# Performance work log

Measured on AMD Instinct MI355X. Metric: run time of the kernel, lower is better.

## Reference

```python
import jax, jax.numpy as jnp
import numpy as np


def _resize_bilinear_align_corners(x, out_size):
    # x: [B, C, h, w] -> [B, C, out_size, out_size], matches F.interpolate(mode='bilinear', align_corners=True)
    def axis_interp(arr, size_in, size_out, axis):
        coords = jnp.linspace(0.0, size_in - 1.0, size_out)
        i0 = jnp.floor(coords).astype(jnp.int32)
        i1 = jnp.minimum(i0 + 1, size_in - 1)
        t = (coords - i0).astype(arr.dtype)
        a0 = jnp.take(arr, i0, axis=axis)
        a1 = jnp.take(arr, i1, axis=axis)
        shape = [1] * arr.ndim
        shape[axis] = size_out
        t = t.reshape(shape)
        return a0 * (1.0 - t) + a1 * t

    B, C, h, w = x.shape
    x = axis_interp(x, h, out_size, 2)
    x = axis_interp(x, w, out_size, 3)
    return x


def _similarity_matrix(x, sp, num):
    # Torch: mean_values[i][j] = mean(x[i][sp_repeated[i] == j], dim=0)
    # Boolean indexing flattens across channels, so this is a SCALAR mean over
    # (channels x segment pixels), broadcast to all C channels.
    B, C, H, W = x.shape
    xs = x.sum(axis=1).reshape(B, H * W)          # sum over channels, per pixel
    ids = sp.reshape(B, H * W)
    seg_sum = jax.vmap(
        lambda v, i: jax.ops.segment_sum(v, i, num_segments=num))(xs, ids)
    cnt = jax.vmap(
        lambda i: jax.ops.segment_sum(jnp.ones(i.shape, x.dtype), i,
                                      num_segments=num))(ids)
    m = seg_sum / (cnt * C)                        # [B, num] scalar mean per segment
    # diff vector over channels has identical entries -> norm(diff)/sqrt(C) == |m_i - m_j|
    return 1.0 - jnp.abs(m[:, :, None] - m[:, None, :])  # [B, num, num]


def reference(input, feature, sp, num):
    feature = _resize_bilinear_align_corners(feature, input.shape[-1])
    mat1 = _similarity_matrix(input, sp, num)
    mat2 = _similarity_matrix(feature, sp, num)
    return jnp.mean(jnp.abs(mat1 - mat2))


def setup_inputs() -> dict:
    key = jax.random.key(0)
    k1, k2, k3 = jax.random.split(key, 3)
    B, C_in, H, W = 8, 64, 256, 256
    C_feat, hf, wf = 256, 64, 64
    num = 256
    return {
        "input": jax.random.normal(k1, (B, C_in, H, W), dtype=jnp.float32),
        "feature": jax.random.normal(k2, (B, C_feat, hf, wf), dtype=jnp.float32),
        "sp": jax.random.randint(k3, (B, 1, H, W), 0, num, dtype=jnp.int32),
        "num": num,
    }
```

## Files before the change

### kernel.cpp

```cpp
#include <hip/hip_runtime.h>

#define NB 8
#define C_IN 64
#define HW 65536
#define CF 256
#define FHW 4096
#define NSEG 256


__global__ void featsum_kernel(const float* __restrict__ feat,
                               float* __restrict__ featsum) {
    int b = blockIdx.y, cg = blockIdx.z;
    int p = blockIdx.x * 256 + threadIdx.x;
    const float* f = feat + ((size_t)(b * CF + cg * 32)) * FHW + p;
    float s = 0.f;
#pragma unroll
    for (int c = 0; c < 32; ++c) s += f[(size_t)c * FHW];
    atomicAdd(&featsum[b * FHW + p], s);
}

__global__ __launch_bounds__(256) void main_kernel(
    const float* __restrict__ input, const int* __restrict__ sp,
    const float* __restrict__ featsum, float* __restrict__ seg) {
    __shared__ float fls[FHW];
    __shared__ float bin_in[NSEG], bin_feat[NSEG], bin_cnt[NSEG];
    int b = blockIdx.y;
    int t = threadIdx.x;
    for (int i = t; i < FHW; i += 256) fls[i] = featsum[b * FHW + i];
    bin_in[t] = 0.f; bin_feat[t] = 0.f; bin_cnt[t] = 0.f;
    __syncthreads();

    int p0 = blockIdx.x * 1024 + t * 4;
    int v0 = p0 >> 2;
    const float4* in4 = (const float4*)(input + (size_t)b * C_IN * HW);
    float4 xs = make_float4(0.f, 0.f, 0.f, 0.f);
#pragma unroll
    for (int c = 0; c < C_IN; ++c) {
        float4 v = in4[(size_t)c * (HW / 4) + v0];
        xs.x += v.x; xs.y += v.y; xs.z += v.z; xs.w += v.w;
    }
    int4 sv = ((const int4*)(sp + (size_t)b * HW))[v0];

    int y = p0 >> 8;
    float cy = (float)y * (63.0f / 255.0f);
    int iy = (int)cy; float ty = cy - (float)iy; int iy1 = min(iy + 1, 63);
    float xsv[4] = {xs.x, xs.y, xs.z, xs.w};
    int   ssv[4] = {sv.x, sv.y, sv.z, sv.w};
#pragma unroll
    for (int k = 0; k < 4; ++k) {
        int x = (p0 + k) & 255;
        float cx = (float)x * (63.0f / 255.0f);
        int ix = (int)cx; float tx = cx - (float)ix; int ix1 = min(ix + 1, 63);
        float f00 = fls[iy * 64 + ix],  f10 = fls[iy1 * 64 + ix];
        float f01 = fls[iy * 64 + ix1], f11 = fls[iy1 * 64 + ix1];
        float a0 = f00 * (1.f - ty) + f10 * ty;
        float a1 = f01 * (1.f - ty) + f11 * ty;
        float fs = a0 * (1.f - tx) + a1 * tx;
        int s = ssv[k];
        atomicAdd(&bin_in[s], xsv[k]);
        atomicAdd(&bin_feat[s], fs);
        atomicAdd(&bin_cnt[s], 1.f);
    }
    __syncthreads();
    atomicAdd(&seg[b * NSEG + t], bin_in[t]);
    atomicAdd(&seg[NB * NSEG + b * NSEG + t], bin_feat[t]);
    atomicAdd(&seg[2 * NB * NSEG + b * NSEG + t], bin_cnt[t]);
}

__global__ void pair_kernel(const float* __restrict__ seg,
                            float* __restrict__ pp) {
    __shared__ float m1[NSEG], m2[NSEG];
    __shared__ float wsum[4];
    int b = blockIdx.y, ig = blockIdx.x, t = threadIdx.x;
    float cnt = seg[2 * NB * NSEG + b * NSEG + t];
    m1[t] = seg[b * NSEG + t] / (cnt * 64.0f);
    m2[t] = seg[NB * NSEG + b * NSEG + t] / (cnt * 256.0f);
    __syncthreads();
    int i = ig * 64 + (t & 63);
    int j0 = (t >> 6) * 64;
    float a1 = m1[i], a2 = m2[i];
    float acc = 0.f;
#pragma unroll 8
    for (int jj = 0; jj < 64; ++jj) {
        int j = j0 + jj;
        acc += fabsf(fabsf(a1 - m1[j]) - fabsf(a2 - m2[j]));
    }
    for (int off = 32; off; off >>= 1) acc += __shfl_down(acc, off);
    if ((t & 63) == 0) wsum[t >> 6] = acc;
    __syncthreads();
    if (t == 0) pp[b * 4 + ig] = wsum[0] + wsum[1] + wsum[2] + wsum[3];
}

__global__ void final_kernel(const float* __restrict__ pp,
                             float* __restrict__ out) {
    int t = threadIdx.x;
    float v = (t < 32) ? pp[t] : 0.f;
    for (int off = 32; off; off >>= 1) v += __shfl_down(v, off);
    if (t == 0) out[0] = v / 524288.0f;
}

extern "C" void kernel_launch(void* const* d_in, const int* in_sizes, int n_in,
                              void* d_out, int out_size, void* d_ws, size_t ws_size,
                              hipStream_t stream) {
    const float* input   = (const float*)d_in[0];
    const float* feature = (const float*)d_in[1];
    const int*   sp      = (const int*)d_in[2];
    float* ws = (float*)d_ws;
    float* featsum = ws;
    float* seg     = ws + NB * FHW;
    float* pp      = seg + 3 * NB * NSEG;

    hipMemsetAsync(d_ws, 0, (size_t)(NB * FHW + 3 * NB * NSEG + 32) * sizeof(float), stream);
    featsum_kernel<<<dim3(16, 8, 8), 256, 0, stream>>>(feature, featsum);
    main_kernel<<<dim3(64, 8), 256, 0, stream>>>(input, sp, featsum, seg);
    pair_kernel<<<dim3(4, 8), 256, 0, stream>>>(seg, pp);
    final_kernel<<<1, 64, 0, stream>>>(pp, (float*)d_out);
}
```

Before: 52.89 us.

## Replace global atomics and memset with per-block partial buffers reduced downstream

Global atomicAdd accumulation is replaced with plain stores of per-group and per-block partial results, which removes the hipMemsetAsync launch. The feature channel-sum kernel now loads float4 and writes 8 channel-group partials, and main_kernel adds those partials together when it fills shared memory. main_kernel writes per-block segment bins, and a single 1024-thread pair block per batch reduces the 64 block partials before computing the pairwise term. The cost is redundant partial reads in each main block and more serial reduction work in pair_kernel.

```diff
diff --git a/kernel.cpp b/kernel.cpp
--- a/kernel.cpp
+++ b/kernel.cpp
@@ -6,32 +6,46 @@
 #define CF 256
 #define FHW 4096
 #define NSEG 256
+#define NGRP 8
+#define MBLK 64
 
 
 __global__ void featsum_kernel(const float* __restrict__ feat,
-                               float* __restrict__ featsum) {
-    int b = blockIdx.y, cg = blockIdx.z;
-    int p = blockIdx.x * 256 + threadIdx.x;
-    const float* f = feat + ((size_t)(b * CF + cg * 32)) * FHW + p;
-    float s = 0.f;
+                               float* __restrict__ partial) {
+    int b = blockIdx.y, g = blockIdx.z;
+    int q = blockIdx.x * 256 + threadIdx.x;
+    const float4* f4 = (const float4*)(feat + ((size_t)(b * CF + g * 32)) * FHW);
+    float4 s = make_float4(0.f, 0.f, 0.f, 0.f);
 #pragma unroll
-    for (int c = 0; c < 32; ++c) s += f[(size_t)c * FHW];
-    atomicAdd(&featsum[b * FHW + p], s);
+    for (int c = 0; c < 32; ++c) {
+        float4 v = f4[(size_t)c * (FHW / 4) + q];
+        s.x += v.x; s.y += v.y; s.z += v.z; s.w += v.w;
+    }
+    ((float4*)partial)[(size_t)(b * NGRP + g) * (FHW / 4) + q] = s;
 }
 
 __global__ __launch_bounds__(256) void main_kernel(
     const float* __restrict__ input, const int* __restrict__ sp,
-    const float* __restrict__ featsum, float* __restrict__ seg) {
+    const float* __restrict__ partial, float* __restrict__ seg_part) {
     __shared__ float fls[FHW];
-    __shared__ float bin_in[NSEG], bin_feat[NSEG], bin_cnt[NSEG];
+    __shared__ float bin[3][NSEG];
     int b = blockIdx.y;
     int t = threadIdx.x;
-    for (int i = t; i < FHW; i += 256) fls[i] = featsum[b * FHW + i];
-    bin_in[t] = 0.f; bin_feat[t] = 0.f; bin_cnt[t] = 0.f;
+    const float4* p4 = (const float4*)(partial + (size_t)b * NGRP * FHW);
+    for (int i = t; i < FHW / 4; i += 256) {
+        float4 s = p4[i];
+#pragma unroll
+        for (int g = 1; g < NGRP; ++g) {
+            float4 v = p4[g * (FHW / 4) + i];
+            s.x += v.x; s.y += v.y; s.z += v.z; s.w += v.w;
+        }
+        ((float4*)fls)[i] = s;
+    }
+    bin[0][t] = 0.f; bin[1][t] = 0.f; bin[2][t] = 0.f;
     __syncthreads();
 
     int p0 = blockIdx.x * 1024 + t * 4;
-    int v0 = p0 >> 2;
+    int v0 = blockIdx.x * 256 + t;
     const float4* in4 = (const float4*)(input + (size_t)b * C_IN * HW);
     float4 xs = make_float4(0.f, 0.f, 0.f, 0.f);
 #pragma unroll
@@ -57,27 +71,39 @@
         float a1 = f01 * (1.f - ty) + f11 * ty;
         float fs = a0 * (1.f - tx) + a1 * tx;
         int s = ssv[k];
-        atomicAdd(&bin_in[s], xsv[k]);
-        atomicAdd(&bin_feat[s], fs);
-        atomicAdd(&bin_cnt[s], 1.f);
+        atomicAdd(&bin[0][s], xsv[k]);
+        atomicAdd(&bin[1][s], fs);
+        atomicAdd(&bin[2][s], 1.f);
     }
     __syncthreads();
-    atomicAdd(&seg[b * NSEG + t], bin_in[t]);
-    atomicAdd(&seg[NB * NSEG + b * NSEG + t], bin_feat[t]);
-    atomicAdd(&seg[2 * NB * NSEG + b * NSEG + t], bin_cnt[t]);
+    float* sb = seg_part + (size_t)(b * MBLK + blockIdx.x) * 3 * NSEG;
+    sb[t]            = bin[0][t];
+    sb[NSEG + t]     = bin[1][t];
+    sb[2 * NSEG + t] = bin[2][t];
 }
 
-__global__ void pair_kernel(const float* __restrict__ seg,
-                            float* __restrict__ pp) {
+__global__ __launch_bounds__(1024) void pair_kernel(
+    const float* __restrict__ seg_part, float* __restrict__ pp) {
+    __shared__ float s3[3 * NSEG];
     __shared__ float m1[NSEG], m2[NSEG];
-    __shared__ float wsum[4];
-    int b = blockIdx.y, ig = blockIdx.x, t = threadIdx.x;
-    float cnt = seg[2 * NB * NSEG + b * NSEG + t];
-    m1[t] = seg[b * NSEG + t] / (cnt * 64.0f);
-    m2[t] = seg[NB * NSEG + b * NSEG + t] / (cnt * 256.0f);
+    __shared__ float red[16];
+    int b = blockIdx.x, t = threadIdx.x;
+    if (t < 3 * NSEG) {
+        float s = 0.f;
+        const float* base = seg_part + (size_t)b * MBLK * 3 * NSEG + t;
+#pragma unroll 8
+        for (int k = 0; k < MBLK; ++k) s += base[(size_t)k * 3 * NSEG];
+        s3[t] = s;
+    }
     __syncthreads();
-    int i = ig * 64 + (t & 63);
-    int j0 = (t >> 6) * 64;
+    if (t < NSEG) {
+        float cnt = s3[2 * NSEG + t];
+        m1[t] = s3[t] / (cnt * 64.0f);
+        m2[t] = s3[NSEG + t] / (cnt * 256.0f);
+    }
+    __syncthreads();
+    int i = t & 255;
+    int j0 = (t >> 8) * 64;
     float a1 = m1[i], a2 = m2[i];
     float acc = 0.f;
 #pragma unroll 8
@@ -85,17 +111,24 @@
         int j = j0 + jj;
         acc += fabsf(fabsf(a1 - m1[j]) - fabsf(a2 - m2[j]));
     }
+#pragma unroll
     for (int off = 32; off; off >>= 1) acc += __shfl_down(acc, off);
-    if ((t & 63) == 0) wsum[t >> 6] = acc;
+    if ((t & 63) == 0) red[t >> 6] = acc;
     __syncthreads();
-    if (t == 0) pp[b * 4 + ig] = wsum[0] + wsum[1] + wsum[2] + wsum[3];
+    if (t == 0) {
+        float s = 0.f;
+#pragma unroll
+        for (int w = 0; w < 16; ++w) s += red[w];
+        pp[b] = s;
+    }
 }
 
 __global__ void final_kernel(const float* __restrict__ pp,
                              float* __restrict__ out) {
     int t = threadIdx.x;
-    float v = (t < 32) ? pp[t] : 0.f;
-    for (int off = 32; off; off >>= 1) v += __shfl_down(v, off);
+    float v = (t < NB) ? pp[t] : 0.f;
+#pragma unroll
+    for (int off = 4; off; off >>= 1) v += __shfl_down(v, off);
     if (t == 0) out[0] = v / 524288.0f;
 }
 
@@ -106,13 +139,12 @@
     const float* feature = (const float*)d_in[1];
     const int*   sp      = (const int*)d_in[2];
     float* ws = (float*)d_ws;
-    float* featsum = ws;
-    float* seg     = ws + NB * FHW;
-    float* pp      = seg + 3 * NB * NSEG;
+    float* partial  = ws;
+    float* seg_part = ws + (size_t)NB * NGRP * FHW;
+    float* pp       = seg_part + (size_t)NB * MBLK * 3 * NSEG;
 
-    hipMemsetAsync(d_ws, 0, (size_t)(NB * FHW + 3 * NB * NSEG + 32) * sizeof(float), stream);
-    featsum_kernel<<<dim3(16, 8, 8), 256, 0, stream>>>(feature, featsum);
-    main_kernel<<<dim3(64, 8), 256, 0, stream>>>(input, sp, featsum, seg);
-    pair_kernel<<<dim3(4, 8), 256, 0, stream>>>(seg, pp);
+    featsum_kernel<<<dim3(4, 8, 8), 256, 0, stream>>>(feature, partial);
+    main_kernel<<<dim3(MBLK, 8), 256, 0, stream>>>(input, sp, partial, seg_part);
+    pair_kernel<<<dim3(8), 1024, 0, stream>>>(seg_part, pp);
     final_kernel<<<1, 64, 0, stream>>>(pp, (float*)d_out);
 }
```

New measurement: 49.79 us. 1.06x faster.
